# Performance work log

Hardware: AMD Instinct MI355X
Metric: run time of the kernel (lower is better)

## Reference

```python
import jax, jax.numpy as jnp
import numpy as np

MODES = 12
WIDTH = 32
M_FREQ = 2 * MODES * (2 * MODES - 1)  # 552


def _gelu(x):
    return jax.nn.gelu(x, approximate=False)  # torch F.gelu default = exact erf


def _build_vfwd(xp, yp):
    # xp, yp: [B, N], already shifted so global min == 0 (in-place subtract in VFT)
    xs = xp * (6.28 / jnp.max(xp))
    ys = yp * (6.28 / jnp.max(yp))
    kx = jnp.concatenate([jnp.arange(MODES), jnp.arange(-MODES, 0)]).astype(xs.dtype)        # [24]
    ky = jnp.concatenate([jnp.arange(MODES), jnp.arange(-(MODES - 1), 0)]).astype(xs.dtype)  # [23]
    # torch layout: X_mat[b, i, n] = kx[i % 24], Y_mat[b, i, n] = ky[i // 24]
    KX = jnp.tile(kx, 2 * MODES - 1)   # [552]
    KY = jnp.repeat(ky, 2 * MODES)     # [552]
    phase = KX[None, :, None] * xs[:, None, :] + KY[None, :, None] * ys[:, None, :]  # [B,552,N]
    n_pts = xs.shape[1]
    scale = np.float32(np.sqrt(2.0) / np.sqrt(n_pts))
    return jnp.exp(-1j * phase).astype(jnp.complex64) * scale


def _spectral_conv(h, Vf, w1, w2):
    # h: [B, C, N] real; Vf: [B, 552, N] complex; w1/w2: [C, C, 12, 12] complex
    B, C, N = h.shape
    # forward NUDFT: (x.permute -> bmm -> permute) == einsum
    x_ft = jnp.einsum('bmn,bcn->bcm', Vf, h.astype(jnp.complex64))       # [B,C,552]
    x_ft = x_ft.reshape(B, C, 2 * MODES, 2 * MODES - 1)                  # [B,C,24,23]
    top = jnp.einsum('bixy,ioxy->boxy', x_ft[:, :, :MODES, :MODES], w1)  # [B,C,12,12]
    bot = jnp.einsum('bixy,ioxy->boxy', x_ft[:, :, -MODES:, :MODES], w2)
    out_ft = jnp.concatenate([top, bot], axis=2)                         # rows :12 and -12: cover all 24
    flat = out_ft.reshape(B, C, 2 * MODES * MODES)                       # [B,C,288]
    # conjugate-flip symmetry completion (note: torch flips dims -1 AND -2, i.e. channels too)
    tail = jnp.conj(jnp.flip(flat[..., 2 * MODES:], axis=(-2, -1)))      # [B,C,264]
    full = jnp.concatenate([flat, tail], axis=-1)                        # [B,C,552]
    # inverse NUDFT: V_inv = conj(V_fwd)^T
    out = jnp.einsum('bmn,bcm->bcn', jnp.conj(Vf), full)                 # [B,C,N]
    return out.real


def setup_inputs() -> dict:
    B, N = 16, 4096
    key = jax.random.key(0)
    ks = jax.random.split(key, 12)
    scale = 1.0 / (WIDTH * WIDTH)
    inp = {
        'pos': jax.random.uniform(ks[0], (B, N, 2), dtype=jnp.float32),
        'fc0_w': jax.random.normal(ks[1], (2, WIDTH), dtype=jnp.float32) / np.sqrt(2.0),
        'fc0_b': jnp.zeros((WIDTH,), jnp.float32),
        'sw1r': scale * jax.random.uniform(ks[2], (4, WIDTH, WIDTH, MODES, MODES), dtype=jnp.float32),
        'sw1i': scale * jax.random.uniform(ks[3], (4, WIDTH, WIDTH, MODES, MODES), dtype=jnp.float32),
        'sw2r': scale * jax.random.uniform(ks[4], (4, WIDTH, WIDTH, MODES, MODES), dtype=jnp.float32),
        'sw2i': scale * jax.random.uniform(ks[5], (4, WIDTH, WIDTH, MODES, MODES), dtype=jnp.float32),
        'cw': jax.random.normal(ks[6], (4, WIDTH, WIDTH), dtype=jnp.float32) / np.sqrt(WIDTH),
        'cb': jnp.zeros((4, WIDTH), jnp.float32),
        'fc1_w': jax.random.normal(ks[7], (WIDTH, 128), dtype=jnp.float32) / np.sqrt(WIDTH),
        'fc1_b': jnp.zeros((128,), jnp.float32),
        'fc2_w': jax.random.normal(ks[8], (128, 1), dtype=jnp.float32) / np.sqrt(128.0),
        'fc2_b': jnp.zeros((1,), jnp.float32),
    }
    return inp


def reference(pos, fc0_w, fc0_b, sw1r, sw1i, sw2r, sw2i, cw, cb, fc1_w, fc1_b, fc2_w, fc2_b):
    # VFT __init__ subtracts the global min IN PLACE, so fc0 sees the shifted coords
    xp = pos[:, :, 0] - jnp.min(pos[:, :, 0])
    yp = pos[:, :, 1] - jnp.min(pos[:, :, 1])
    Vf = _build_vfwd(xp, yp)                       # [B,552,N]
    xin = jnp.stack([xp, yp], axis=-1)             # [B,N,2]
    h = xin @ fc0_w + fc0_b                        # [B,N,32]
    h = h.transpose(0, 2, 1)                       # [B,32,N]
    for l in range(4):
        w1 = sw1r[l] + 1j * sw1i[l]
        w2 = sw2r[l] + 1j * sw2i[l]
        h1 = _spectral_conv(h, Vf, w1, w2)
        h2 = jnp.einsum('oc,bcn->bon', cw[l], h) + cb[l][None, :, None]  # Conv1d k=1
        h = h1 + h2
        if l < 3:
            h = _gelu(h)
    h = h.transpose(0, 2, 1)                       # [B,N,32]
    h = _gelu(h @ fc1_w + fc1_b)                   # [B,N,128]
    return h @ fc2_w + fc2_b                       # [B,N,1]
```

## Files before the change

### kernel.cpp

```cpp
#include <hip/hip_runtime.h>
#include <hip/hip_bf16.h>
#include <math.h>

#define BB 16
#define NPT 4096
#define CH 32
#define MX 24
#define MYK 23
#define NF 288
#define NS 16
#define KTI 9
#define SCALE_V 0.022097086912079608f
#define INV_S 45.25483399593904f

typedef __attribute__((ext_vector_type(8))) short s8v;
typedef __attribute__((ext_vector_type(4))) float f4v;
typedef __attribute__((ext_vector_type(4))) unsigned u32x4;
typedef unsigned short u16;
typedef unsigned int u32;

#define MF(A, B, C) C = __builtin_amdgcn_mfma_f32_16x16x32_bf16(A, B, C, 0, 0, 0)

static __device__ __forceinline__ float gelu_f(float x) {
  return 0.5f * x * (1.0f + erff(x * 0.70710678118654752f));
}

static __device__ __forceinline__ void bsplit(float v, u16 &hi, u16 &lo) {
  __hip_bfloat16 h = __float2bfloat16(v);
  hi = __builtin_bit_cast(u16, h);
  float r = v - __bfloat162float(h);
  lo = __builtin_bit_cast(u16, __float2bfloat16(r));
}

static __device__ __forceinline__ void split2(float v0, float v1, u32 &hw, u32 &lw) {
  u32 b0 = __builtin_bit_cast(u32, v0) & 0xFFFF0000u;
  u32 b1 = __builtin_bit_cast(u32, v1) & 0xFFFF0000u;
  float r0 = v0 - __builtin_bit_cast(float, b0);
  float r1 = v1 - __builtin_bit_cast(float, b1);
  hw = __builtin_amdgcn_perm(b1, b0, 0x07060302u);
  lw = __builtin_amdgcn_perm(__builtin_bit_cast(u32, r1), __builtin_bit_cast(u32, r0), 0x07060302u);
}

__global__ void k_minmax1(const float* __restrict__ pos, float* __restrict__ partials) {
  int t = threadIdx.x;
  float mnx = 1e30f, mxx = -1e30f, mny = 1e30f, mxy = -1e30f;
  for (int idx = blockIdx.x * 256 + t; idx < BB * NPT; idx += 64 * 256) {
    float2 p = ((const float2*)pos)[idx];
    mnx = fminf(mnx, p.x); mxx = fmaxf(mxx, p.x);
    mny = fminf(mny, p.y); mxy = fmaxf(mxy, p.y);
  }
  for (int o = 32; o > 0; o >>= 1) {
    mnx = fminf(mnx, __shfl_down(mnx, o));
    mxx = fmaxf(mxx, __shfl_down(mxx, o));
    mny = fminf(mny, __shfl_down(mny, o));
    mxy = fmaxf(mxy, __shfl_down(mxy, o));
  }
  __shared__ float sm[4][4];
  if ((t & 63) == 0) { int wv = t >> 6; sm[wv][0] = mnx; sm[wv][1] = mxx; sm[wv][2] = mny; sm[wv][3] = mxy; }
  __syncthreads();
  if (t == 0) {
    for (int w = 1; w < 4; ++w) {
      mnx = fminf(mnx, sm[w][0]); mxx = fmaxf(mxx, sm[w][1]);
      mny = fminf(mny, sm[w][2]); mxy = fmaxf(mxy, sm[w][3]);
    }
    partials[blockIdx.x * 4 + 0] = mnx; partials[blockIdx.x * 4 + 1] = mxx;
    partials[blockIdx.x * 4 + 2] = mny; partials[blockIdx.x * 4 + 3] = mxy;
  }
}

__global__ void k_minmax2(const float* __restrict__ partials, float* __restrict__ scal) {
  int t = threadIdx.x;
  float mnx = partials[t * 4 + 0], mxx = partials[t * 4 + 1];
  float mny = partials[t * 4 + 2], mxy = partials[t * 4 + 3];
  for (int o = 32; o > 0; o >>= 1) {
    mnx = fminf(mnx, __shfl_down(mnx, o));
    mxx = fmaxf(mxx, __shfl_down(mxx, o));
    mny = fminf(mny, __shfl_down(mny, o));
    mxy = fmaxf(mxy, __shfl_down(mxy, o));
  }
  if (t == 0) {
    scal[0] = mnx; scal[1] = mny;
    scal[2] = 6.28f / (mxx - mnx);
    scal[3] = 6.28f / (mxy - mny);
  }
}

__global__ __launch_bounds__(256) void k_setup(const float* __restrict__ pos,
    const float* __restrict__ fc0w, const float* __restrict__ fc0b,
    const float* __restrict__ scal,
    float2* __restrict__ ExI, float2* __restrict__ EyI, float* __restrict__ hA) {
  int p = blockIdx.x * 256 + threadIdx.x;
  int b = p >> 12, n = p & (NPT - 1);
  float px = pos[2 * p], py = pos[2 * p + 1];
  float xp = px - scal[0], yp = py - scal[1];
  float xs = xp * scal[2], ys = yp * scal[3];
  #pragma unroll
  for (int c = 0; c < CH; ++c)
    hA[((b * CH + c) << 12) + n] = fmaf(xp, fc0w[c], fmaf(yp, fc0w[32 + c], fc0b[c]));
  float cx, sx_; sincosf(xs, &sx_, &cx);
  ExI[(b * MX + 0) * NPT + n] = make_float2(SCALE_V, 0.f);
  float pr = SCALE_V, pi = 0.f;
  for (int k = 1; k <= 12; ++k) {
    float nr = pr * cx + pi * sx_;
    float ni = pi * cx - pr * sx_;
    pr = nr; pi = ni;
    if (k < 12) {
      ExI[(b * MX + k) * NPT + n] = make_float2(pr, pi);
      ExI[(b * MX + 24 - k) * NPT + n] = make_float2(pr, -pi);
    } else {
      ExI[(b * MX + 12) * NPT + n] = make_float2(pr, -pi);
    }
  }
  float cy, sy_; sincosf(ys, &sy_, &cy);
  EyI[(b * MYK + 0) * NPT + n] = make_float2(1.f, 0.f);
  float qr = 1.f, qi = 0.f;
  for (int k = 1; k <= 11; ++k) {
    float nr = qr * cy + qi * sy_;
    float ni = qi * cy - qr * sy_;
    qr = nr; qi = ni;
    EyI[(b * MYK + k) * NPT + n] = make_float2(qr, qi);
    EyI[(b * MYK + 23 - k) * NPT + n] = make_float2(qr, -qi);
  }
}

__global__ __launch_bounds__(256) void k_wtcw(const float* __restrict__ sw1r, const float* __restrict__ sw1i,
    const float* __restrict__ sw2r, const float* __restrict__ sw2i,
    float* __restrict__ wtr, float* __restrict__ wti,
    const float* __restrict__ cw, u16* __restrict__ cwb) {
  if (blockIdx.x >= 256) {
    int l = blockIdx.x - 256, t = threadIdx.x;
    for (int idx = t; idx < 1024; idx += 256) {
      int ct = idx >> 9, rem = idx & 511, lane = rem >> 3, e = rem & 7;
      int o = ct * 16 + (lane & 15);
      int c2 = (lane >> 4) * 8 + e;
      float v = cw[l * 1024 + o * 32 + c2];
      u16 hi, lo; bsplit(v, hi, lo);
      cwb[((l * 2 + 0) * 2 + ct) * 512 + lane * 8 + e] = hi;
      cwb[((l * 2 + 1) * 2 + ct) * 512 + lane * 8 + e] = lo;
    }
    return;
  }
  int l = blockIdx.x >> 6, i = (blockIdx.x >> 1) & 31, a = blockIdx.x & 1;
  __shared__ float S[2][32][145];
  const float* src1 = (a ? sw1i : sw1r) + ((l * 32 + i) * 32) * 144;
  const float* src2 = (a ? sw2i : sw2r) + ((l * 32 + i) * 32) * 144;
  for (int e = threadIdx.x; e < 32 * 144; e += 256) {
    S[0][e / 144][e % 144] = src1[e];
    S[1][e / 144][e % 144] = src2[e];
  }
  __syncthreads();
  float* dstbuf = a ? wti : wtr;
  for (int f0 = 0; f0 < 288; f0 += 8) {
    int f = f0 + (threadIdx.x >> 5), o = threadIdx.x & 31;
    float v = (f < 144) ? S[0][o][f] : S[1][o][f - 144];
    dstbuf[((l * 288 + f) * 32 + i) * 32 + o] = v;
  }
}

__global__ __launch_bounds__(384) void k_fwd_m(const float* __restrict__ hin,
    const float2* __restrict__ ExI, const float2* __restrict__ EyI,
    float* __restrict__ xfr, float* __restrict__ xfi) {
  const int b = blockIdx.y, s = blockIdx.z;
  const int t = threadIdx.x, w = t >> 6, l = t & 63;
  const int mtile = blockIdx.x * 6 + w;
  const int lr = l & 15, lg = l >> 4;
  const int f_row = mtile * 16 + lr;
  const int mp = 23 * (f_row / 12) + (f_row % 12);
  const int irow = mp % 24, jrow = mp / 24;

  __shared__ float2 exs[MX][34];
  __shared__ u16 bh[2][64][8];
  __shared__ u16 bl[2][64][8];

  f4v aR0 = {0.f,0.f,0.f,0.f}, aI0 = {0.f,0.f,0.f,0.f};
  f4v aR1 = {0.f,0.f,0.f,0.f}, aI1 = {0.f,0.f,0.f,0.f};
  const int nbase = s << 8;

  const float2* eyrow = EyI + ((size_t)(b * MYK + jrow)) * NPT + lg * 8;

  const int rS = t >> 5, nS = t & 31;
  const int cA = t >> 4, nrA = (t & 15) * 2;
  const int cB = (t + 384) >> 4, nrB = ((t + 384) & 15) * 2;
  const int ctA = cA >> 4, lnA = ((nrA >> 3) << 4) | (cA & 15), eeA = nrA & 7;
  const int ctB = cB >> 4, lnB = ((nrB >> 3) << 4) | (cB & 15), eeB = nrB & 7;

  float2 apx0, apx1, ah2, ah3;
  float2 bpx0, bpx1, bh2, bh3;

#define PFL(kt, px0_, px1_, h2_, h3_) { \
    const int n0_ = nbase + ((kt) << 5); \
    px0_ = ExI[(b * MX + rS) * NPT + n0_ + nS]; \
    px1_ = ExI[(b * MX + rS + 12) * NPT + n0_ + nS]; \
    h2_ = *(const float2*)&hin[((b * CH + cA) << 12) + n0_ + nrA]; \
    if (t < 128) h3_ = *(const float2*)&hin[((b * CH + cB) << 12) + n0_ + nrB]; }

#define STG(px0_, px1_, h2_, h3_) { \
    exs[rS][nS] = px0_; exs[rS + 12][nS] = px1_; \
    u32 hw_, lw_; split2(h2_.x, h2_.y, hw_, lw_); \
    *(u32*)&bh[ctA][lnA][eeA] = hw_; *(u32*)&bl[ctA][lnA][eeA] = lw_; \
    if (t < 128) { u32 hw2_, lw2_; split2(h3_.x, h3_.y, hw2_, lw2_); \
      *(u32*)&bh[ctB][lnB][eeB] = hw2_; *(u32*)&bl[ctB][lnB][eeB] = lw2_; } }

  auto COMPUTE = [&](int n0_) {
    u32x4 rh, rl, ih, il;
    #pragma unroll
    for (int e2 = 0; e2 < 4; ++e2) {
      float4 qx = *(const float4*)&exs[irow][lg * 8 + 2 * e2];
      float4 qy = *(const float4*)&eyrow[n0_ + 2 * e2];
      float vr0 = qx.x * qy.x - qx.y * qy.y;
      float vi0 = qx.x * qy.y + qx.y * qy.x;
      float vr1 = qx.z * qy.z - qx.w * qy.w;
      float vi1 = qx.z * qy.w + qx.w * qy.z;
      u32 w0, w1, w2, w3;
      split2(vr0, vr1, w0, w1);
      split2(vi0, vi1, w2, w3);
      rh[e2] = w0; rl[e2] = w1; ih[e2] = w2; il[e2] = w3;
    }
    s8v arh = __builtin_bit_cast(s8v, rh), arl = __builtin_bit_cast(s8v, rl);
    s8v aih = __builtin_bit_cast(s8v, ih), ail = __builtin_bit_cast(s8v, il);
    s8v b0h = *(const s8v*)(&bh[0][l][0]);
    s8v b0l = *(const s8v*)(&bl[0][l][0]);
    s8v b1h = *(const s8v*)(&bh[1][l][0]);
    s8v b1l = *(const s8v*)(&bl[1][l][0]);
    MF(arh, b0h, aR0); MF(arh, b0l, aR0); MF(arl, b0h, aR0);
    MF(aih, b0h, aI0); MF(aih, b0l, aI0); MF(ail, b0h, aI0);
    MF(arh, b1h, aR1); MF(arh, b1l, aR1); MF(arl, b1h, aR1);
    MF(aih, b1h, aI1); MF(aih, b1l, aI1); MF(ail, b1h, aI1);
  };

  PFL(0, apx0, apx1, ah2, ah3);
  PFL(1, bpx0, bpx1, bh2, bh3);
  #pragma unroll
  for (int kt2 = 0; kt2 < 4; ++kt2) {
    __syncthreads();
    STG(apx0, apx1, ah2, ah3);
    if (kt2 < 3) PFL(2 * kt2 + 2, apx0, apx1, ah2, ah3);
    __syncthreads();
    COMPUTE(nbase + ((2 * kt2) << 5));
    __syncthreads();
    STG(bpx0, bpx1, bh2, bh3);
    if (kt2 < 3) PFL(2 * kt2 + 3, bpx0, bpx1, bh2, bh3);
    __syncthreads();
    COMPUTE(nbase + ((2 * kt2 + 1) << 5));
  }
#undef PFL
#undef STG
  #pragma unroll
  for (int r = 0; r < 4; ++r) {
    int fo = mtile * 16 + lg * 4 + r;
    int base = ((s * BB + b) * NF + fo) * CH + lr;
    xfr[base] = aR0[r]; xfr[base + 16] = aR1[r];
    xfi[base] = aI0[r]; xfi[base + 16] = aI1[r];
  }
}

static __device__ __forceinline__ void fbs(u16* __restrict__ fb, int b, int f, int c, int ri, float v) {
  int kt = f >> 5, kr = f & 31;
  int ct = c >> 4, ln = ((kr >> 3) << 4) | (c & 15), e = kr & 7;
  u16 hi, lo; bsplit(v, hi, lo);
  int off = (b * KTI + kt) * 4096 + ri * 2048 + ct * 512 + ln * 8 + e;
  fb[off] = hi;
  fb[off + 1024] = lo;
}

__global__ __launch_bounds__(256) void k_mix(const float* __restrict__ xfr, const float* __restrict__ xfi,
    const float* __restrict__ wtr, const float* __restrict__ wti,
    u16* __restrict__ fullB, int l) {
  const int f = blockIdx.x, b = blockIdx.y;
  const int t = threadIdx.x;
  __shared__ float xr_[CH], xi_[CH];
  __shared__ float rr[8][33], ri_[8][33];
  if (t < 64) {
    int i = t & 31, isIm = t >> 5;
    const float* src = isIm ? xfi : xfr;
    float v = 0.f;
    #pragma unroll
    for (int s = 0; s < NS; ++s) v += src[((s * BB + b) * NF + f) * CH + i];
    if (isIm) xi_[i] = v; else xr_[i] = v;
  }
  __syncthreads();
  {
    int o = t & 31, ig = t >> 5;
    float pr = 0.f, pi = 0.f;
    const float* wr_base = wtr + (l * NF + f) * CH * CH;
    const float* wi_base = wti + (l * NF + f) * CH * CH;
    #pragma unroll
    for (int q = 0; q < 4; ++q) {
      int i = ig * 4 + q;
      float xr = xr_[i], xi = xi_[i];
      float w1 = wr_base[i * CH + o], w2 = wi_base[i * CH + o];
      pr += xr * w1 - xi * w2;
      pi += xr * w2 + xi * w1;
    }
    rr[ig][o] = pr; ri_[ig][o] = pi;
  }
  __syncthreads();
  if (t < 64) {
    int o2 = t & 31, isIm = t >> 5;
    float v = 0.f;
    #pragma unroll
    for (int g = 0; g < 8; ++g) v += isIm ? ri_[g][o2] : rr[g][o2];
    fbs(fullB, b, f, o2, isIm, v);
  }
}

__global__ __launch_bounds__(256) void k_inv_m(const float* __restrict__ hin,
    const float2* __restrict__ ExI, const float2* __restrict__ EyI,
    const u16* __restrict__ fullB,
    const u16* __restrict__ cwb, const float* __restrict__ cb,
    float* __restrict__ hout, int l, int doGelu) {
  const int b = blockIdx.y;
  const int n0 = blockIdx.x << 6;
  const int t = threadIdx.x, w = t >> 6, l6 = t & 63;
  const int lr = l6 & 15, lg = l6 >> 4;

  __shared__ float2 exT[64][26];
  __shared__ u16 bfr[4096];

  const int nloc = w * 16 + lr;

  uint4 qa0, qa1, qb0, qb1;
#define LDNA(kt) { const uint4* s_ = (const uint4*)(fullB + (size_t)(b * KTI + (kt)) * 4096); qa0 = s_[t]; qa1 = s_[t + 256]; }
#define LDNB(kt) { const uint4* s_ = (const uint4*)(fullB + (size_t)(b * KTI + (kt)) * 4096); qb0 = s_[t]; qb1 = s_[t + 256]; }
#define WRTA { uint4* d_ = (uint4*)bfr; d_[t] = qa0; d_[t + 256] = qa1; }
#define WRTB { uint4* d_ = (uint4*)bfr; d_[t] = qb0; d_[t + 256] = qb1; }
  LDNA(0); LDNB(1);

  for (int e = t; e < MX * 64; e += 256) { int i = e >> 6, nn = e & 63; exT[nn][i] = ExI[(b * MX + i) * NPT + n0 + nn]; }

  float2 eyv[KTI];
  #pragma unroll
  for (int kt = 0; kt < KTI; ++kt) {
    int mb = (kt << 5) + (lg << 3);
    int j = (mb * 2731) >> 16;
    eyv[kt] = EyI[(b * MYK + j) * NPT + n0 + nloc];
  }

  s8v ah_c, al_c;
  {
    float hv[8];
    #pragma unroll
    for (int e = 0; e < 8; ++e)
      hv[e] = hin[((b * CH + lg * 8 + e) << 12) + n0 + nloc];
    u32x4 hh, hl2;
    #pragma unroll
    for (int e2 = 0; e2 < 4; ++e2) {
      u32 a_, b_;
      split2(hv[2 * e2], hv[2 * e2 + 1], a_, b_);
      hh[e2] = a_; hl2[e2] = b_;
    }
    ah_c = __builtin_bit_cast(s8v, hh);
    al_c = __builtin_bit_cast(s8v, hl2);
  }

  const u16* cwp = cwb + l * 2048;
  s8v cwh0 = *(const s8v*)(cwp + 0    + l6 * 8);
  s8v cwh1 = *(const s8v*)(cwp + 512  + l6 * 8);
  s8v cwl0 = *(const s8v*)(cwp + 1024 + l6 * 8);
  s8v cwl1 = *(const s8v*)(cwp + 1536 + l6 * 8);

  f4v P0 = {0,0,0,0}, P1 = {0,0,0,0}, B0 = {0,0,0,0}, B1 = {0,0,0,0};
  MF(ah_c, cwh0, P0); MF(ah_c, cwl0, P0); MF(al_c, cwh0, P0);
  MF(ah_c, cwh1, P1); MF(ah_c, cwl1, P1); MF(al_c, cwh1, P1);
  f4v S1a0 = P0, S1a1 = P1, S1b0 = {0,0,0,0}, S1b1 = {0,0,0,0};

  auto CMP = [&](int kt) {
    const int mbase = (kt << 5) + (lg << 3);
    const int j = (mbase * 2731) >> 16;
    const int i0 = mbase - 24 * j;
    const float2 ey = eyv[kt];
    u32x4 rh, rl, ih, il;
    #pragma unroll
    for (int e2 = 0; e2 < 4; ++e2) {
      float4 q = *(const float4*)&exT[nloc][i0 + 2 * e2];
      float vr0 = q.x * ey.x - q.y * ey.y;
      float vi0 = q.x * ey.y + q.y * ey.x;
      float vr1 = q.z * ey.x - q.w * ey.y;
      float vi1 = q.z * ey.y + q.w * ey.x;
      u32 w0, w1, w2, w3;
      split2(vr0, vr1, w0, w1);
      split2(vi0, vi1, w2, w3);
      rh[e2] = w0; rl[e2] = w1; ih[e2] = w2; il[e2] = w3;
    }
    s8v arh = __builtin_bit_cast(s8v, rh), arl = __builtin_bit_cast(s8v, rl);
    s8v aih = __builtin_bit_cast(s8v, ih), ail = __builtin_bit_cast(s8v, il);
    u32x4 nh = rh ^ 0x80008000u, nl2 = rl ^ 0x80008000u;
    s8v narh = __builtin_bit_cast(s8v, nh), narl = __builtin_bit_cast(s8v, nl2);

    const u16* bp = bfr;
    s8v Frh0 = *(const s8v*)(bp + 0    + l6 * 8);
    s8v Frh1 = *(const s8v*)(bp + 512  + l6 * 8);
    s8v Frl0 = *(const s8v*)(bp + 1024 + l6 * 8);
    s8v Frl1 = *(const s8v*)(bp + 1536 + l6 * 8);
    s8v Fih0 = *(const s8v*)(bp + 2048 + l6 * 8);
    s8v Fih1 = *(const s8v*)(bp + 2560 + l6 * 8);
    s8v Fil0 = *(const s8v*)(bp + 3072 + l6 * 8);
    s8v Fil1 = *(const s8v*)(bp + 3584 + l6 * 8);
    MF(arh, Frh0, P0); MF(arh, Frl0, P0); MF(arl, Frh0, P0);
    MF(aih, Fih0, P0); MF(aih, Fil0, P0); MF(ail, Fih0, P0);
    MF(arh, Frh1, P1); MF(arh, Frl1, P1); MF(arl, Frh1, P1);
    MF(aih, Fih1, P1); MF(aih, Fil1, P1); MF(ail, Fih1, P1);
    MF(aih, Frh0, B0); MF(aih, Frl0, B0); MF(ail, Frh0, B0);
    MF(narh, Fih0, B0); MF(narh, Fil0, B0); MF(narl, Fih0, B0);
    MF(aih, Frh1, B1); MF(aih, Frl1, B1); MF(ail, Frh1, B1);
    MF(narh, Fih1, B1); MF(narh, Fil1, B1); MF(narl, Fih1, B1);
    if (kt == 0) {
      s8v z = {0,0,0,0,0,0,0,0};
      bool live = (lg < 3);
      s8v zrh = live ? arh : z, zrl = live ? arl : z;
      s8v zih = live ? aih : z, zil = live ? ail : z;
      s8v znrh = live ? narh : z, znrl = live ? narl : z;
      MF(zrh, Frh0, S1a0); MF(zrh, Frl0, S1a0); MF(zrl, Frh0, S1a0);
      MF(zih, Fih0, S1a0); MF(zih, Fil0, S1a0); MF(zil, Fih0, S1a0);
      MF(zrh, Frh1, S1a1); MF(zrh, Frl1, S1a1); MF(zrl, Frh1, S1a1);
      MF(zih, Fih1, S1a1); MF(zih, Fil1, S1a1); MF(zil, Fih1, S1a1);
      MF(zih, Frh0, S1b0); MF(zih, Frl0, S1b0); MF(zil, Frh0, S1b0);
      MF(znrh, Fih0, S1b0); MF(znrh, Fil0, S1b0); MF(znrl, Fih0, S1b0);
      MF(zih, Frh1, S1b1); MF(zih, Frl1, S1b1); MF(zil, Frh1, S1b1);
      MF(znrh, Fih1, S1b1); MF(znrh, Fil1, S1b1); MF(znrl, Fih1, S1b1);
    }
  };

  #pragma unroll
  for (int kt2 = 0; kt2 < 4; ++kt2) {
    __syncthreads(); WRTA; LDNA(2 * kt2 + 2);
    __syncthreads(); CMP(2 * kt2);
    __syncthreads(); WRTB; if (kt2 < 3) LDNB(2 * kt2 + 3);
    __syncthreads(); CMP(2 * kt2 + 1);
  }
  __syncthreads(); WRTA;
  __syncthreads(); CMP(8);
#undef LDNA
#undef LDNB
#undef WRTA
#undef WRTB

  float cb0 = cb[l * CH + lr];
  float cb1 = cb[l * CH + 16 + lr];
  #pragma unroll
  for (int r = 0; r < 4; ++r) {
    int nn = w * 16 + lg * 4 + r;
    float2 e1 = exT[nn][1];
    float cs = e1.x * INV_S, sn = -e1.y * INV_S;
    float a20 = P0[r] - S1a0[r], a21 = P1[r] - S1a1[r];
    float b20 = B0[r] - S1b0[r], b21 = B1[r] - S1b1[r];
    float U0r = cs * a20 + sn * b20;
    float U1r = cs * a21 + sn * b21;
    float u1s = __shfl_xor(U1r, 15, 64);
    float u0s = __shfl_xor(U0r, 15, 64);
    float v0 = P0[r] + u1s + cb0;
    float v1 = P1[r] + u0s + cb1;
    if (doGelu) { v0 = gelu_f(v0); v1 = gelu_f(v1); }
    hout[((b * CH + lr) << 12) + n0 + nn] = v0;
    hout[((b * CH + 16 + lr) << 12) + n0 + nn] = v1;
  }
}

__global__ __launch_bounds__(256) void k_final(const float* __restrict__ hin,
    const float* __restrict__ fc1w, const float* __restrict__ fc1b,
    const float* __restrict__ fc2w, const float* __restrict__ fc2b, float* __restrict__ out) {
  __shared__ float w1s[CH * 128];
  __shared__ float b1s[128], w2s[128];
  int t = threadIdx.x;
  for (int e = t; e < CH * 128; e += 256) w1s[e] = fc1w[e];
  if (t < 128) { b1s[t] = fc1b[t]; w2s[t] = fc2w[t]; }
  __syncthreads();
  int p = blockIdx.x * 256 + t;
  int b = p >> 12, n = p & (NPT - 1);
  float h[CH];
  #pragma unroll
  for (int c2 = 0; c2 < CH; ++c2) h[c2] = hin[((b * CH + c2) << 12) + n];
  float o = fc2b[0];
  for (int k0 = 0; k0 < 128; k0 += 4) {
    float4 a = *(const float4*)&b1s[k0];
    #pragma unroll
    for (int c2 = 0; c2 < CH; ++c2) {
      float4 wv = *(const float4*)&w1s[c2 * 128 + k0];
      a.x += h[c2] * wv.x; a.y += h[c2] * wv.y;
      a.z += h[c2] * wv.z; a.w += h[c2] * wv.w;
    }
    float4 g = *(const float4*)&w2s[k0];
    o += gelu_f(a.x) * g.x + gelu_f(a.y) * g.y + gelu_f(a.z) * g.z + gelu_f(a.w) * g.w;
  }
  out[p] = o;
}

extern "C" void kernel_launch(void* const* d_in, const int* in_sizes, int n_in,
                              void* d_out, int out_size, void* d_ws, size_t ws_size,
                              hipStream_t stream) {
  const float* pos   = (const float*)d_in[0];
  const float* fc0_w = (const float*)d_in[1];
  const float* fc0_b = (const float*)d_in[2];
  const float* sw1r  = (const float*)d_in[3];
  const float* sw1i  = (const float*)d_in[4];
  const float* sw2r  = (const float*)d_in[5];
  const float* sw2i  = (const float*)d_in[6];
  const float* cw    = (const float*)d_in[7];
  const float* cb    = (const float*)d_in[8];
  const float* fc1_w = (const float*)d_in[9];
  const float* fc1_b = (const float*)d_in[10];
  const float* fc2_w = (const float*)d_in[11];
  const float* fc2_b = (const float*)d_in[12];
  float* out = (float*)d_out;
  float* ws = (float*)d_ws;

  size_t off = 0;
  float* partials = ws;                 off += 256;
  float* scal = ws + off;               off += 16;
  float2* ExI = (float2*)(ws + off);    off += (size_t)BB * MX * NPT * 2;
  float2* EyI = (float2*)(ws + off);    off += (size_t)BB * MYK * NPT * 2;
  float* hA  = ws + off;                off += (size_t)BB * CH * NPT;
  float* hB  = ws + off;                off += (size_t)BB * CH * NPT;
  float* xfr = ws + off;                off += (size_t)NS * BB * NF * CH;
  float* xfi = ws + off;                off += (size_t)NS * BB * NF * CH;
  u16*  fullB = (u16*)(ws + off);       off += (size_t)BB * KTI * 4096 / 2;
  float* wtr = ws + off;                off += (size_t)4 * NF * CH * CH;
  float* wti = ws + off;                off += (size_t)4 * NF * CH * CH;
  u16*  cwb = (u16*)(ws + off);         off += 4096;

  k_minmax1<<<64, 256, 0, stream>>>(pos, partials);
  k_minmax2<<<1, 64, 0, stream>>>(partials, scal);
  k_setup<<<(BB * NPT) / 256, 256, 0, stream>>>(pos, fc0_w, fc0_b, scal, ExI, EyI, hA);
  k_wtcw<<<260, 256, 0, stream>>>(sw1r, sw1i, sw2r, sw2i, wtr, wti, cw, cwb);

  for (int l = 0; l < 4; ++l) {
    const float* hin = (l & 1) ? hB : hA;
    float* hout = (l & 1) ? hA : hB;
    k_fwd_m<<<dim3(3, BB, NS), 384, 0, stream>>>(hin, ExI, EyI, xfr, xfi);
    k_mix<<<dim3(NF, BB), 256, 0, stream>>>(xfr, xfi, wtr, wti, fullB, l);
    k_inv_m<<<dim3(64, BB), 256, 0, stream>>>(hin, ExI, EyI, fullB, cwb, cb,
                                              hout, l, (l < 3) ? 1 : 0);
  }
  k_final<<<(BB * NPT) / 256, 256, 0, stream>>>(hA, fc1_w, fc1_b, fc2_w, fc2_b, out);
}
```

Baseline: 284.4 us.

## Split inverse NUDFT K-loop across two wave groups with LDS reduction

```diff
diff --git a/kernel.cpp b/kernel.cpp
--- a/kernel.cpp
+++ b/kernel.cpp
@@ -304,7 +304,7 @@
   }
 }
 
-__global__ __launch_bounds__(256) void k_inv_m(const float* __restrict__ hin,
+__global__ __launch_bounds__(512) void k_inv_m(const float* __restrict__ hin,
     const float2* __restrict__ ExI, const float2* __restrict__ EyI,
     const u16* __restrict__ fullB,
     const u16* __restrict__ cwb, const float* __restrict__ cb,
@@ -313,31 +313,29 @@
   const int n0 = blockIdx.x << 6;
   const int t = threadIdx.x, w = t >> 6, l6 = t & 63;
   const int lr = l6 & 15, lg = l6 >> 4;
+  const int wk = w >> 2, wr = w & 3;
 
   __shared__ float2 exT[64][26];
-  __shared__ u16 bfr[4096];
-
-  const int nloc = w * 16 + lr;
-
-  uint4 qa0, qa1, qb0, qb1;
-#define LDNA(kt) { const uint4* s_ = (const uint4*)(fullB + (size_t)(b * KTI + (kt)) * 4096); qa0 = s_[t]; qa1 = s_[t + 256]; }
-#define LDNB(kt) { const uint4* s_ = (const uint4*)(fullB + (size_t)(b * KTI + (kt)) * 4096); qb0 = s_[t]; qb1 = s_[t + 256]; }
-#define WRTA { uint4* d_ = (uint4*)bfr; d_[t] = qa0; d_[t + 256] = qa1; }
-#define WRTB { uint4* d_ = (uint4*)bfr; d_[t] = qb0; d_[t + 256] = qb1; }
-  LDNA(0); LDNB(1);
-
-  for (int e = t; e < MX * 64; e += 256) { int i = e >> 6, nn = e & 63; exT[nn][i] = ExI[(b * MX + i) * NPT + n0 + nn]; }
-
-  float2 eyv[KTI];
+  __shared__ float red[256][20];
+
+  const int nloc = wr * 16 + lr;
+
+  for (int e = t; e < MX * 64; e += 512) { int i = e >> 6, nn = e & 63; exT[nn][i] = ExI[(b * MX + i) * NPT + n0 + nn]; }
+
+  const int ktbeg = wk ? 4 : 0, ktend = wk ? KTI : 4;
+  float2 eyv[5];
   #pragma unroll
-  for (int kt = 0; kt < KTI; ++kt) {
-    int mb = (kt << 5) + (lg << 3);
-    int j = (mb * 2731) >> 16;
-    eyv[kt] = EyI[(b * MYK + j) * NPT + n0 + nloc];
-  }
-
-  s8v ah_c, al_c;
-  {
+  for (int q = 0; q < 5; ++q) {
+    int kt = ktbeg + q;
+    if (kt < ktend) {
+      int mb = (kt << 5) + (lg << 3);
+      int j = (mb * 2731) >> 16;
+      eyv[q] = EyI[(b * MYK + j) * NPT + n0 + nloc];
+    }
+  }
+
+  s8v ah_c, al_c, cwh0, cwh1, cwl0, cwl1;
+  if (wk == 0) {
     float hv[8];
     #pragma unroll
     for (int e = 0; e < 8; ++e)
@@ -351,32 +349,51 @@
     }
     ah_c = __builtin_bit_cast(s8v, hh);
     al_c = __builtin_bit_cast(s8v, hl2);
-  }
-
-  const u16* cwp = cwb + l * 2048;
-  s8v cwh0 = *(const s8v*)(cwp + 0    + l6 * 8);
-  s8v cwh1 = *(const s8v*)(cwp + 512  + l6 * 8);
-  s8v cwl0 = *(const s8v*)(cwp + 1024 + l6 * 8);
-  s8v cwl1 = *(const s8v*)(cwp + 1536 + l6 * 8);
+    const u16* cwp = cwb + l * 2048;
+    cwh0 = *(const s8v*)(cwp + 0    + l6 * 8);
+    cwh1 = *(const s8v*)(cwp + 512  + l6 * 8);
+    cwl0 = *(const s8v*)(cwp + 1024 + l6 * 8);
+    cwl1 = *(const s8v*)(cwp + 1536 + l6 * 8);
+  }
+
+  __syncthreads();
 
   f4v P0 = {0,0,0,0}, P1 = {0,0,0,0}, B0 = {0,0,0,0}, B1 = {0,0,0,0};
-  MF(ah_c, cwh0, P0); MF(ah_c, cwl0, P0); MF(al_c, cwh0, P0);
-  MF(ah_c, cwh1, P1); MF(ah_c, cwl1, P1); MF(al_c, cwh1, P1);
-  f4v S1a0 = P0, S1a1 = P1, S1b0 = {0,0,0,0}, S1b1 = {0,0,0,0};
-
-  auto CMP = [&](int kt) {
+  f4v S1a0 = {0,0,0,0}, S1a1 = {0,0,0,0}, S1b0 = {0,0,0,0}, S1b1 = {0,0,0,0};
+  if (wk == 0) {
+    MF(ah_c, cwh0, P0); MF(ah_c, cwl0, P0); MF(al_c, cwh0, P0);
+    MF(ah_c, cwh1, P1); MF(ah_c, cwl1, P1); MF(al_c, cwh1, P1);
+    S1a0 = P0; S1a1 = P1;
+  }
+
+  const u16* fbb = fullB + (size_t)(b * KTI) * 4096 + l6 * 8;
+
+  #pragma unroll
+  for (int q = 0; q < 5; ++q) {
+    int kt = ktbeg + q;
+    if (kt >= ktend) break;
+    const u16* bp = fbb + kt * 4096;
+    s8v Frh0 = *(const s8v*)(bp + 0);
+    s8v Frh1 = *(const s8v*)(bp + 512);
+    s8v Frl0 = *(const s8v*)(bp + 1024);
+    s8v Frl1 = *(const s8v*)(bp + 1536);
+    s8v Fih0 = *(const s8v*)(bp + 2048);
+    s8v Fih1 = *(const s8v*)(bp + 2560);
+    s8v Fil0 = *(const s8v*)(bp + 3072);
+    s8v Fil1 = *(const s8v*)(bp + 3584);
+
     const int mbase = (kt << 5) + (lg << 3);
     const int j = (mbase * 2731) >> 16;
     const int i0 = mbase - 24 * j;
-    const float2 ey = eyv[kt];
+    const float2 ey = eyv[q];
     u32x4 rh, rl, ih, il;
     #pragma unroll
     for (int e2 = 0; e2 < 4; ++e2) {
-      float4 q = *(const float4*)&exT[nloc][i0 + 2 * e2];
-      float vr0 = q.x * ey.x - q.y * ey.y;
-      float vi0 = q.x * ey.y + q.y * ey.x;
-      float vr1 = q.z * ey.x - q.w * ey.y;
-      float vi1 = q.z * ey.y + q.w * ey.x;
+      float4 qq = *(const float4*)&exT[nloc][i0 + 2 * e2];
+      float vr0 = qq.x * ey.x - qq.y * ey.y;
+      float vi0 = qq.x * ey.y + qq.y * ey.x;
+      float vr1 = qq.z * ey.x - qq.w * ey.y;
+      float vi1 = qq.z * ey.y + qq.w * ey.x;
       u32 w0, w1, w2, w3;
       split2(vr0, vr1, w0, w1);
       split2(vi0, vi1, w2, w3);
@@ -387,15 +404,6 @@
     u32x4 nh = rh ^ 0x80008000u, nl2 = rl ^ 0x80008000u;
     s8v narh = __builtin_bit_cast(s8v, nh), narl = __builtin_bit_cast(s8v, nl2);
 
-    const u16* bp = bfr;
-    s8v Frh0 = *(const s8v*)(bp + 0    + l6 * 8);
-    s8v Frh1 = *(const s8v*)(bp + 512  + l6 * 8);
-    s8v Frl0 = *(const s8v*)(bp + 1024 + l6 * 8);
-    s8v Frl1 = *(const s8v*)(bp + 1536 + l6 * 8);
-    s8v Fih0 = *(const s8v*)(bp + 2048 + l6 * 8);
-    s8v Fih1 = *(const s8v*)(bp + 2560 + l6 * 8);
-    s8v Fil0 = *(const s8v*)(bp + 3072 + l6 * 8);
-    s8v Fil1 = *(const s8v*)(bp + 3584 + l6 * 8);
     MF(arh, Frh0, P0); MF(arh, Frl0, P0); MF(arl, Frh0, P0);
     MF(aih, Fih0, P0); MF(aih, Fil0, P0); MF(ail, Fih0, P0);
     MF(arh, Frh1, P1); MF(arh, Frl1, P1); MF(arl, Frh1, P1);
@@ -419,40 +427,42 @@
       MF(zih, Frh1, S1b1); MF(zih, Frl1, S1b1); MF(zil, Frh1, S1b1);
       MF(znrh, Fih1, S1b1); MF(znrh, Fil1, S1b1); MF(znrl, Fih1, S1b1);
     }
-  };
-
-  #pragma unroll
-  for (int kt2 = 0; kt2 < 4; ++kt2) {
-    __syncthreads(); WRTA; LDNA(2 * kt2 + 2);
-    __syncthreads(); CMP(2 * kt2);
-    __syncthreads(); WRTB; if (kt2 < 3) LDNB(2 * kt2 + 3);
-    __syncthreads(); CMP(2 * kt2 + 1);
-  }
-  __syncthreads(); WRTA;
-  __syncthreads(); CMP(8);
-#undef LDNA
-#undef LDNB
-#undef WRTA
-#undef WRTB
-
-  float cb0 = cb[l * CH + lr];
-  float cb1 = cb[l * CH + 16 + lr];
-  #pragma unroll
-  for (int r = 0; r < 4; ++r) {
-    int nn = w * 16 + lg * 4 + r;
-    float2 e1 = exT[nn][1];
-    float cs = e1.x * INV_S, sn = -e1.y * INV_S;
-    float a20 = P0[r] - S1a0[r], a21 = P1[r] - S1a1[r];
-    float b20 = B0[r] - S1b0[r], b21 = B1[r] - S1b1[r];
-    float U0r = cs * a20 + sn * b20;
-    float U1r = cs * a21 + sn * b21;
-    float u1s = __shfl_xor(U1r, 15, 64);
-    float u0s = __shfl_xor(U0r, 15, 64);
-    float v0 = P0[r] + u1s + cb0;
-    float v1 = P1[r] + u0s + cb1;
-    if (doGelu) { v0 = gelu_f(v0); v1 = gelu_f(v1); }
-    hout[((b * CH + lr) << 12) + n0 + nn] = v0;
-    hout[((b * CH + 16 + lr) << 12) + n0 + nn] = v1;
+  }
+
+  if (wk == 1) {
+    int row = wr * 64 + l6;
+    *(f4v*)&red[row][0]  = P0;
+    *(f4v*)&red[row][4]  = P1;
+    *(f4v*)&red[row][8]  = B0;
+    *(f4v*)&red[row][12] = B1;
+  }
+  __syncthreads();
+  if (wk == 0) {
+    int row = wr * 64 + l6;
+    P0 += *(const f4v*)&red[row][0];
+    P1 += *(const f4v*)&red[row][4];
+    B0 += *(const f4v*)&red[row][8];
+    B1 += *(const f4v*)&red[row][12];
+
+    float cb0 = cb[l * CH + lr];
+    float cb1 = cb[l * CH + 16 + lr];
+    #pragma unroll
+    for (int r = 0; r < 4; ++r) {
+      int nn = wr * 16 + lg * 4 + r;
+      float2 e1 = exT[nn][1];
+      float cs = e1.x * INV_S, sn = -e1.y * INV_S;
+      float a20 = P0[r] - S1a0[r], a21 = P1[r] - S1a1[r];
+      float b20 = B0[r] - S1b0[r], b21 = B1[r] - S1b1[r];
+      float U0r = cs * a20 + sn * b20;
+      float U1r = cs * a21 + sn * b21;
+      float u1s = __shfl_xor(U1r, 15, 64);
+      float u0s = __shfl_xor(U0r, 15, 64);
+      float v0 = P0[r] + u1s + cb0;
+      float v1 = P1[r] + u0s + cb1;
+      if (doGelu) { v0 = gelu_f(v0); v1 = gelu_f(v1); }
+      hout[((b * CH + lr) << 12) + n0 + nn] = v0;
+      hout[((b * CH + 16 + lr) << 12) + n0 + nn] = v1;
+    }
   }
 }
 
@@ -528,7 +538,7 @@
     float* hout = (l & 1) ? hA : hB;
     k_fwd_m<<<dim3(3, BB, NS), 384, 0, stream>>>(hin, ExI, EyI, xfr, xfi);
     k_mix<<<dim3(NF, BB), 256, 0, stream>>>(xfr, xfi, wtr, wti, fullB, l);
-    k_inv_m<<<dim3(64, BB), 256, 0, stream>>>(hin, ExI, EyI, fullB, cwb, cb,
+    k_inv_m<<<dim3(64, BB), 512, 0, stream>>>(hin, ExI, EyI, fullB, cwb, cb,
                                               hout, l, (l < 3) ? 1 : 0);
   }
   k_final<<<(BB * NPT) / 256, 256, 0, stream>>>(hA, fc1_w, fc1_b, fc2_w, fc2_b, out);
```

After: 283.3 us. No clear change (-0.4%).
